# Kernel optimization log

Measured on AMD Instinct MI355X. Metric: run time of the kernel, lower is better.

Reference implementation:

```python
import jax, jax.numpy as jnp
import numpy as np
import math

H = 16          # num_heads
EPS = 1e-5      # LayerNorm eps (torch default)


def setup_inputs() -> dict:
    key = jax.random.key(0)
    ks = jax.random.split(key, 4)
    B, T, D = 2, 2048, 1024
    s = 1.0 / math.sqrt(D)
    return {
        "x": jax.random.normal(ks[0], (B, T, D), dtype=jnp.float32),
        "ln_g": jnp.ones((D,), jnp.float32),
        "ln_b": jnp.zeros((D,), jnp.float32),
        "Wq": jax.random.normal(ks[1], (D, D), jnp.float32) * s,
        "bq": jnp.zeros((D,), jnp.float32),
        "Wk": jax.random.normal(ks[2], (D, D), jnp.float32) * s,
        "bk": jnp.zeros((D,), jnp.float32),
        "Wv": jax.random.normal(ks[3], (D, D), jnp.float32) * s,
        "bv": jnp.zeros((D,), jnp.float32),
    }


def reference(x, ln_g, ln_b, Wq, bq, Wk, bk, Wv, bv):
    B, T, D = x.shape
    # LayerNorm (shared across the three projections, computed once)
    mu = jnp.mean(x, axis=-1, keepdims=True)
    var = jnp.mean(jnp.square(x - mu), axis=-1, keepdims=True)
    xn = (x - mu) * jax.lax.rsqrt(var + EPS) * ln_g + ln_b
    # Q/K/V projections -> [B, T, H, Dh]
    q = (xn @ Wq + bq).reshape(B, T, H, D // H)
    k = (xn @ Wk + bk).reshape(B, T, H, D // H)
    v = (xn @ Wv + bv).reshape(B, T, H, D // H)
    # QK^T scores [B, n, m, h], scaled by sqrt(head_dim)
    scale = 1.0 / math.sqrt(D // H)
    attn = jnp.einsum('bnhd,bmhd->bnmh', q, k) * scale
    # softmax over key axis (dim=2), dropout p=0 is identity
    w = jax.nn.softmax(attn, axis=2)
    # weighted sum of values, merge heads
    y = jnp.einsum('bnmh,bmhd->bnhd', w, v).reshape(B, T, D)
    return y
```

## Files before the change

kernel.cpp:

```cpp
#include <hip/hip_runtime.h>
#include <hip/hip_bf16.h>


typedef __attribute__((ext_vector_type(8)))  short short8;
typedef __attribute__((ext_vector_type(4)))  float f32x4;
typedef __attribute__((ext_vector_type(2)))  float f32x2;
typedef __attribute__((ext_vector_type(16))) float f32x16;
typedef __attribute__((ext_vector_type(2)))  unsigned int uint2v;

#define D_MODEL 1024
#define T_SEQ   2048
#define NHEAD   16
#define HDIM    64

#define LOG2E 1.4426950408889634f

__device__ __forceinline__ unsigned short f2bf(float x) {
    unsigned int u = __float_as_uint(x);
    u = (u + 0x7fffu + ((u >> 16) & 1u)) >> 16;
    return (unsigned short)u;
}

#if defined(__has_builtin)
#if __has_builtin(__builtin_amdgcn_permlane32_swap)
#define HAVE_PERMSWAP 1
#endif
#endif

__device__ __forceinline__ uint2v permswap(unsigned a, unsigned b) {
#ifdef HAVE_PERMSWAP
    return __builtin_amdgcn_permlane32_swap(a, b, false, false);
#else
    uint2v r;
    const unsigned as = (unsigned)__shfl_xor((int)a, 32, 64);
    const unsigned bs = (unsigned)__shfl_xor((int)b, 32, 64);
    const bool hi = (threadIdx.x & 32) != 0;
    r[0] = hi ? bs : a;
    r[1] = hi ? b  : as;
    return r;
#endif
}

__device__ __forceinline__ void w8(unsigned short* p, const uint4 v) {
    uint2 a; a.x = v.x; a.y = v.y;
    uint2 b; b.x = v.z; b.y = v.w;
    *(uint2*)p = a;
    *(uint2*)(p + 4) = b;
}

__device__ __forceinline__ short8 read8(const unsigned short* p) {
    union { unsigned u[4]; short8 s; } r;
    const uint2 a = *(const uint2*)p;
    const uint2 b = *(const uint2*)(p + 4);
    r.u[0] = a.x; r.u[1] = a.y; r.u[2] = b.x; r.u[3] = b.y;
    return r.s;
}

__global__ __launch_bounds__(256) void ln_kernel(
    const float* __restrict__ x, const float* __restrict__ gam,
    const float* __restrict__ bet, unsigned short* __restrict__ xn)
{
    const int row = blockIdx.x;
    const int t = threadIdx.x;
    const float4 v = ((const float4*)(x + (size_t)row * D_MODEL))[t];
    float s  = v.x + v.y + v.z + v.w;
    float s2 = v.x * v.x + v.y * v.y + v.z * v.z + v.w * v.w;
#pragma unroll
    for (int off = 32; off; off >>= 1) {
        s  += __shfl_down(s,  off, 64);
        s2 += __shfl_down(s2, off, 64);
    }
    __shared__ float red[8];
    const int lane = t & 63, wave = t >> 6;
    if (lane == 0) { red[wave] = s; red[4 + wave] = s2; }
    __syncthreads();
    s  = red[0] + red[1] + red[2] + red[3];
    s2 = red[4] + red[5] + red[6] + red[7];
    const float mu   = s * (1.f / D_MODEL);
    const float var  = s2 * (1.f / D_MODEL) - mu * mu;
    const float rstd = rsqrtf(var + 1e-5f);
    const float4 gv = ((const float4*)gam)[t];
    const float4 bv = ((const float4*)bet)[t];
    ushort4 o;
    o.x = f2bf((v.x - mu) * rstd * gv.x + bv.x);
    o.y = f2bf((v.y - mu) * rstd * gv.y + bv.y);
    o.z = f2bf((v.z - mu) * rstd * gv.z + bv.z);
    o.w = f2bf((v.w - mu) * rstd * gv.w + bv.w);
    ((ushort4*)(xn + (size_t)row * D_MODEL))[t] = o;
}

__global__ __launch_bounds__(256) void wcast_kernel(
    const float* __restrict__ Wq, const float* __restrict__ Wk,
    const float* __restrict__ Wv, unsigned short* __restrict__ Wt)
{
    const float* W = (blockIdx.z == 0) ? Wq : (blockIdx.z == 1) ? Wk : Wv;
    unsigned short* out = Wt + (size_t)blockIdx.z * D_MODEL * D_MODEL;
    __shared__ float tile[32][33];
    const int n0 = blockIdx.x * 32, k0 = blockIdx.y * 32;
#pragma unroll
    for (int i = threadIdx.y; i < 32; i += 8)
        tile[i][threadIdx.x] = W[(size_t)(k0 + i) * D_MODEL + n0 + threadIdx.x];
    __syncthreads();
#pragma unroll
    for (int i = threadIdx.y; i < 32; i += 8)
        out[(size_t)(n0 + i) * D_MODEL + k0 + threadIdx.x] = f2bf(tile[threadIdx.x][i]);
}

__global__ __launch_bounds__(256) void qkv_gemm_kernel(
    const unsigned short* __restrict__ xn, const unsigned short* __restrict__ Wt,
    const float* __restrict__ bq, const float* __restrict__ bk, const float* __restrict__ bv,
    unsigned short* __restrict__ qo, unsigned short* __restrict__ ko, unsigned short* __restrict__ vo)
{
    const int which = blockIdx.x >> 3;
    const unsigned short* Bw = Wt + (size_t)which * (D_MODEL * D_MODEL);
    const float* bias   = (which == 0) ? bq : (which == 1) ? bk : bv;
    unsigned short* out = (which == 0) ? qo : (which == 1) ? ko : vo;
    const float scale   = (which == 0) ? (0.125f * LOG2E) : 1.0f;
    const int m0 = blockIdx.y * 128, n0 = (blockIdx.x & 7) * 128;

    __shared__ unsigned short As[128][32];
    __shared__ unsigned short Bs[128][32];

    const int tid = threadIdx.x;
    const int lane = tid & 63, wave = tid >> 6;
    const int wr = wave >> 1, wc = wave & 1;
    const int g = lane >> 4, c = lane & 15;

    const int srow = (lane >> 2);
    const int scol = (lane & 3) * 8;

    f32x4 acc[4][4] = {};

    for (int kt = 0; kt < D_MODEL; kt += 32) {
        __syncthreads();
#pragma unroll
        for (int i = 0; i < 2; ++i) {
            const int r = wave * 32 + i * 16;
            const unsigned short* ga = xn + (size_t)(m0 + r + srow) * D_MODEL + kt + scol;
            __builtin_amdgcn_global_load_lds(
                (const __attribute__((address_space(1))) unsigned int*)ga,
                (__attribute__((address_space(3))) unsigned int*)(&As[r][0]), 16, 0, 0);
            const unsigned short* gb = Bw + (size_t)(n0 + r + srow) * D_MODEL + kt + scol;
            __builtin_amdgcn_global_load_lds(
                (const __attribute__((address_space(1))) unsigned int*)gb,
                (__attribute__((address_space(3))) unsigned int*)(&Bs[r][0]), 16, 0, 0);
        }
        __syncthreads();

        short8 af[4], bf[4];
#pragma unroll
        for (int i = 0; i < 4; ++i) {
            af[i] = *(const short8*)(&As[wr * 64 + i * 16 + c][g * 8]);
            bf[i] = *(const short8*)(&Bs[wc * 64 + i * 16 + c][g * 8]);
        }
#pragma unroll
        for (int i = 0; i < 4; ++i)
#pragma unroll
            for (int j = 0; j < 4; ++j)
                acc[i][j] = __builtin_amdgcn_mfma_f32_16x16x32_bf16(af[i], bf[j], acc[i][j], 0, 0, 0);
    }

#pragma unroll
    for (int j = 0; j < 4; ++j) {
        const int n = n0 + wc * 64 + j * 16 + c;
        const float bn = bias[n];
        const int h = n >> 6, dh = n & 63;
#pragma unroll
        for (int i = 0; i < 4; ++i) {
#pragma unroll
            for (int r = 0; r < 4; ++r) {
                const int m = m0 + wr * 64 + i * 16 + g * 4 + r;
                const int bb = m >> 11, t = m & 2047;
                out[((size_t)(bb * NHEAD + h) * T_SEQ + t) * HDIM + dh] =
                    f2bf((acc[i][j][r] + bn) * scale);
            }
        }
    }
}

__global__ __launch_bounds__(256) void vtrans_kernel(
    const unsigned short* __restrict__ vh, unsigned short* __restrict__ vt)
{
    __shared__ unsigned short tile[64][65];
    const int t0 = blockIdx.x * 64;
    const int bh = blockIdx.y;
    const unsigned short* src = vh + (size_t)bh * T_SEQ * HDIM;
    unsigned short* dst = vt + (size_t)bh * HDIM * T_SEQ;
    const int r0 = threadIdx.x >> 3, d0 = (threadIdx.x & 7) * 8;
#pragma unroll
    for (int it = 0; it < 2; ++it) {
        const int r = r0 + it * 32;
        const uint4 v = *(const uint4*)(src + (size_t)(t0 + r) * HDIM + d0);
        const unsigned short* vs = (const unsigned short*)&v;
#pragma unroll
        for (int j = 0; j < 8; ++j) tile[r][d0 + j] = vs[j];
    }
    __syncthreads();
#pragma unroll
    for (int it = 0; it < 2; ++it) {
        const int dh = r0 + it * 32;
        unsigned short tmp[8];
#pragma unroll
        for (int j = 0; j < 8; ++j) tmp[j] = tile[d0 + j][dh];
        *(uint4*)(dst + (size_t)dh * T_SEQ + t0 + d0) = *(const uint4*)tmp;
    }
}

__global__ __launch_bounds__(512, 4) void attn_kernel(
    const unsigned short* __restrict__ qb, const unsigned short* __restrict__ kb,
    const unsigned short* __restrict__ vtb, float* __restrict__ out)
{
    const int id  = blockIdx.x;
    const int swz = (id & 7) * 64 + (id >> 3);
    const int qt  = swz & 15;
    const int bh  = swz >> 4;
    const int b = bh >> 4, head = bh & 15;
    const unsigned short* Q  = qb  + (size_t)bh * T_SEQ * HDIM;
    const unsigned short* Kp = kb  + (size_t)bh * T_SEQ * HDIM;
    const unsigned short* Vt = vtb + (size_t)bh * HDIM * T_SEQ;

    __shared__ __align__(16) unsigned short smem[34816];

    const int tid = threadIdx.x, lane = tid & 63, wave = tid >> 6;
    const int grp = wave >> 2, w4 = wave & 3;
    const int q = lane & 31, h = lane >> 5;
    const int kvbase = grp * (T_SEQ / 2);

    const int gtid = tid & 255;
    const int sr = gtid >> 3;
    const int sc = (gtid & 7) * 8;

    unsigned short* gbase = &smem[grp * 17408];

    short8 qf[4];
    {
        const unsigned short* qp = Q + (size_t)(qt * 128 + w4 * 32 + q) * HDIM;
#pragma unroll
        for (int c = 0; c < 4; ++c)
            qf[c] = *(const short8*)(qp + c * 16 + h * 8);
    }

    float l_r = 0.f;
    f32x16 o[2] = {};

    const unsigned short* kp0 = Kp + (size_t)(kvbase + sr) * HDIM + sc;
    const unsigned short* vp0 = Vt + (size_t)sr * T_SEQ + kvbase + sc;
    uint4 kr0 = *(const uint4*)(kp0);
    uint4 kr1 = *(const uint4*)(kp0 + 32 * HDIM);
    uint4 vr0 = *(const uint4*)(vp0);
    uint4 vr1 = *(const uint4*)(vp0 + 32 * T_SEQ);
    w8(gbase + sr * 68 + sc, kr0);
    w8(gbase + (sr + 32) * 68 + sc, kr1);
    w8(gbase + 8704 + sr * 68 + sc, vr0);
    w8(gbase + 8704 + (sr + 32) * 68 + sc, vr1);
    kp0 += 64 * HDIM;
    vp0 += 64;

    int cur = 0;
#pragma unroll 1
    for (int t = 0; t < 16; ++t) {
        const bool more = (t + 1 < 16);
        if (more) {
            kr0 = *(const uint4*)(kp0);
            kr1 = *(const uint4*)(kp0 + 32 * HDIM);
            vr0 = *(const uint4*)(vp0);
            vr1 = *(const uint4*)(vp0 + 32 * T_SEQ);
            kp0 += 64 * HDIM;
            vp0 += 64;
        }
        __syncthreads();
        const unsigned short* kbuf = gbase + cur * 4352;
        const unsigned short* vbuf = gbase + 8704 + cur * 4352;

        f32x16 s0 = {}, s1 = {};
        __builtin_amdgcn_s_setprio(1);
#pragma unroll
        for (int c = 0; c < 4; ++c) {
            const short8 kf0 = read8(kbuf + (size_t)q * 68 + c * 16 + h * 8);
            const short8 kf1 = read8(kbuf + (size_t)(32 + q) * 68 + c * 16 + h * 8);
            s0 = __builtin_amdgcn_mfma_f32_32x32x16_bf16(kf0, qf[c], s0, 0, 0, 0);
            s1 = __builtin_amdgcn_mfma_f32_32x32x16_bf16(kf1, qf[c], s1, 0, 0, 0);
        }
        __builtin_amdgcn_s_setprio(0);

#pragma unroll
        for (int r = 0; r < 16; ++r) { s0[r] = exp2f(s0[r]); }
#pragma unroll
        for (int r = 0; r < 16; ++r) { s1[r] = exp2f(s1[r]); }

        {
            f32x2 u[8];
#pragma unroll
            for (int r = 0; r < 8; ++r) {
                f32x2 a; a[0] = s0[2*r]; a[1] = s0[2*r+1];
                f32x2 bb; bb[0] = s1[2*r]; bb[1] = s1[2*r+1];
                u[r] = a + bb;
            }
            u[0] += u[1]; u[2] += u[3]; u[4] += u[5]; u[6] += u[7];
            u[0] += u[2]; u[4] += u[6];
            u[0] += u[4];
            float rs = u[0][0] + u[0][1];
            rs += __shfl_xor(rs, 32, 64);
            l_r += rs;
        }

        unsigned Wb0[8], Wb1[8];
#pragma unroll
        for (int u = 0; u < 4; ++u) {
            asm("v_cvt_pk_bf16_f32 %0, %1, %2" : "=v"(Wb0[u*2])   : "v"(s0[4*u]),   "v"(s0[4*u+1]));
            asm("v_cvt_pk_bf16_f32 %0, %1, %2" : "=v"(Wb0[u*2+1]) : "v"(s0[4*u+2]), "v"(s0[4*u+3]));
            asm("v_cvt_pk_bf16_f32 %0, %1, %2" : "=v"(Wb1[u*2])   : "v"(s1[4*u]),   "v"(s1[4*u+1]));
            asm("v_cvt_pk_bf16_f32 %0, %1, %2" : "=v"(Wb1[u*2+1]) : "v"(s1[4*u+2]), "v"(s1[4*u+3]));
        }

        short8 pf[4];
#pragma unroll
        for (int m = 0; m < 2; ++m) {
            {
                const uint2v r0 = permswap(Wb0[4*m],     Wb0[4*m + 2]);
                const uint2v r1 = permswap(Wb0[4*m + 1], Wb0[4*m + 3]);
                union { unsigned u[4]; short8 s; } pw;
                pw.u[0] = r0[0]; pw.u[1] = r1[0]; pw.u[2] = r0[1]; pw.u[3] = r1[1];
                pf[m] = pw.s;
            }
            {
                const uint2v r0 = permswap(Wb1[4*m],     Wb1[4*m + 2]);
                const uint2v r1 = permswap(Wb1[4*m + 1], Wb1[4*m + 3]);
                union { unsigned u[4]; short8 s; } pw;
                pw.u[0] = r0[0]; pw.u[1] = r1[0]; pw.u[2] = r0[1]; pw.u[3] = r1[1];
                pf[2 + m] = pw.s;
            }
        }

        __builtin_amdgcn_s_setprio(1);
#pragma unroll
        for (int dt = 0; dt < 2; ++dt) {
#pragma unroll
            for (int cp = 0; cp < 4; ++cp) {
                const short8 vf = read8(vbuf + (size_t)(dt * 32 + q) * 68 + cp * 16 + h * 8);
                o[dt] = __builtin_amdgcn_mfma_f32_32x32x16_bf16(vf, pf[cp], o[dt], 0, 0, 0);
            }
        }
        __builtin_amdgcn_s_setprio(0);

        if (more) {
            unsigned short* kd = gbase + (cur ^ 1) * 4352;
            unsigned short* vd = gbase + 8704 + (cur ^ 1) * 4352;
            w8(kd + sr * 68 + sc, kr0);
            w8(kd + (sr + 32) * 68 + sc, kr1);
            w8(vd + sr * 68 + sc, vr0);
            w8(vd + (sr + 32) * 68 + sc, vr1);
        }
        cur ^= 1;
    }

    __syncthreads();
    float* obuf  = (float*)(void*)smem;
    float* l_lds = ((float*)(void*)smem) + 128 * 68;

    const int qrl = w4 * 32 + q;
    if (grp == 0) {
#pragma unroll
        for (int dt = 0; dt < 2; ++dt)
#pragma unroll
            for (int u = 0; u < 4; ++u) {
                float* dst = obuf + (size_t)qrl * 68 + dt * 32 + 8 * u + 4 * h;
                float2 lo; lo.x = o[dt][4*u];     lo.y = o[dt][4*u + 1];
                float2 hi; hi.x = o[dt][4*u + 2]; hi.y = o[dt][4*u + 3];
                *(float2*)dst = lo;
                *(float2*)(dst + 2) = hi;
            }
        if (h == 0) l_lds[qrl] = l_r;
    }
    __syncthreads();
    if (grp == 1) {
        const float invl = 1.0f / (l_lds[qrl] + l_r);
#pragma unroll
        for (int dt = 0; dt < 2; ++dt)
#pragma unroll
            for (int u = 0; u < 4; ++u) {
                float* dst = obuf + (size_t)qrl * 68 + dt * 32 + 8 * u + 4 * h;
                float2 lo = *(const float2*)dst;
                float2 hi = *(const float2*)(dst + 2);
                lo.x = (lo.x + o[dt][4*u])     * invl;
                lo.y = (lo.y + o[dt][4*u + 1]) * invl;
                hi.x = (hi.x + o[dt][4*u + 2]) * invl;
                hi.y = (hi.y + o[dt][4*u + 3]) * invl;
                *(float2*)dst = lo;
                *(float2*)(dst + 2) = hi;
            }
    }
    __syncthreads();
#pragma unroll
    for (int it = 0; it < 4; ++it) {
        const int row = it * 32 + (tid >> 4);
        const int col = (tid & 15) * 4;
        const float4 v = *(const float4*)(&obuf[(size_t)row * 68 + col]);
        *(float4*)(&out[(size_t)(b * T_SEQ + qt * 128 + row) * D_MODEL + head * HDIM + col]) = v;
    }
}

extern "C" void kernel_launch(void* const* d_in, const int* in_sizes, int n_in,
                              void* d_out, int out_size, void* d_ws, size_t ws_size,
                              hipStream_t stream)
{
    const float* x   = (const float*)d_in[0];
    const float* lng = (const float*)d_in[1];
    const float* lnb = (const float*)d_in[2];
    const float* Wq  = (const float*)d_in[3];
    const float* bq  = (const float*)d_in[4];
    const float* Wk  = (const float*)d_in[5];
    const float* bk  = (const float*)d_in[6];
    const float* Wv  = (const float*)d_in[7];
    const float* bv  = (const float*)d_in[8];
    float* out = (float*)d_out;

    unsigned short* xn = (unsigned short*)d_ws;
    unsigned short* Wt = xn + (size_t)4096 * 1024;
    unsigned short* qh = Wt + (size_t)3 * 1024 * 1024;
    unsigned short* kh = qh + (size_t)4096 * 1024;
    unsigned short* vh = kh + (size_t)4096 * 1024;
    unsigned short* vt = xn;

    ln_kernel<<<4096, 256, 0, stream>>>(x, lng, lnb, xn);
    wcast_kernel<<<dim3(32, 32, 3), dim3(32, 8), 0, stream>>>(Wq, Wk, Wv, Wt);
    qkv_gemm_kernel<<<dim3(24, 32), 256, 0, stream>>>(xn, Wt, bq, bk, bv, qh, kh, vh);
    vtrans_kernel<<<dim3(32, 32), 256, 0, stream>>>(vh, vt);
    attn_kernel<<<512, 512, 0, stream>>>(qh, kh, vt, out);
}
```

Measured before the change: 111.9 us.

## Fuse LN with weight cast, emit transposed V from GEMM, use group barrier

Merges the LayerNorm and weight-cast kernels into one launch. For the V projection the GEMM now swaps its operands (W_v^T times xn^T), so it writes V directly in the head-dim-major layout the attention kernel reads, and the separate transpose kernel is removed. The attention loop's __syncthreads is replaced with an explicit lgkmcnt wait followed by s_barrier. Together these cut two kernel launches and one round trip of V through memory. The V epilogue now writes along t with per-element stores, which may be less coalesced.

```diff
diff --git a/kernel.cpp b/kernel.cpp
--- a/kernel.cpp
+++ b/kernel.cpp
@@ -41,6 +41,12 @@
 #endif
 }
 
+__device__ __forceinline__ void group_barrier() {
+    asm volatile("s_waitcnt lgkmcnt(0)" ::: "memory");
+    __builtin_amdgcn_s_barrier();
+    asm volatile("" ::: "memory");
+}
+
 __device__ __forceinline__ void w8(unsigned short* p, const uint4 v) {
     uint2 a; a.x = v.x; a.y = v.y;
     uint2 b; b.x = v.z; b.y = v.w;
@@ -56,67 +62,74 @@
     return r.s;
 }
 
-__global__ __launch_bounds__(256) void ln_kernel(
+__global__ __launch_bounds__(256) void ln_wcast_kernel(
     const float* __restrict__ x, const float* __restrict__ gam,
-    const float* __restrict__ bet, unsigned short* __restrict__ xn)
-{
-    const int row = blockIdx.x;
-    const int t = threadIdx.x;
-    const float4 v = ((const float4*)(x + (size_t)row * D_MODEL))[t];
-    float s  = v.x + v.y + v.z + v.w;
-    float s2 = v.x * v.x + v.y * v.y + v.z * v.z + v.w * v.w;
-#pragma unroll
-    for (int off = 32; off; off >>= 1) {
-        s  += __shfl_down(s,  off, 64);
-        s2 += __shfl_down(s2, off, 64);
-    }
-    __shared__ float red[8];
-    const int lane = t & 63, wave = t >> 6;
-    if (lane == 0) { red[wave] = s; red[4 + wave] = s2; }
-    __syncthreads();
-    s  = red[0] + red[1] + red[2] + red[3];
-    s2 = red[4] + red[5] + red[6] + red[7];
-    const float mu   = s * (1.f / D_MODEL);
-    const float var  = s2 * (1.f / D_MODEL) - mu * mu;
-    const float rstd = rsqrtf(var + 1e-5f);
-    const float4 gv = ((const float4*)gam)[t];
-    const float4 bv = ((const float4*)bet)[t];
-    ushort4 o;
-    o.x = f2bf((v.x - mu) * rstd * gv.x + bv.x);
-    o.y = f2bf((v.y - mu) * rstd * gv.y + bv.y);
-    o.z = f2bf((v.z - mu) * rstd * gv.z + bv.z);
-    o.w = f2bf((v.w - mu) * rstd * gv.w + bv.w);
-    ((ushort4*)(xn + (size_t)row * D_MODEL))[t] = o;
-}
-
-__global__ __launch_bounds__(256) void wcast_kernel(
+    const float* __restrict__ bet, unsigned short* __restrict__ xn,
     const float* __restrict__ Wq, const float* __restrict__ Wk,
     const float* __restrict__ Wv, unsigned short* __restrict__ Wt)
 {
-    const float* W = (blockIdx.z == 0) ? Wq : (blockIdx.z == 1) ? Wk : Wv;
-    unsigned short* out = Wt + (size_t)blockIdx.z * D_MODEL * D_MODEL;
+    __shared__ float red[8];
     __shared__ float tile[32][33];
-    const int n0 = blockIdx.x * 32, k0 = blockIdx.y * 32;
-#pragma unroll
-    for (int i = threadIdx.y; i < 32; i += 8)
-        tile[i][threadIdx.x] = W[(size_t)(k0 + i) * D_MODEL + n0 + threadIdx.x];
-    __syncthreads();
-#pragma unroll
-    for (int i = threadIdx.y; i < 32; i += 8)
-        out[(size_t)(n0 + i) * D_MODEL + k0 + threadIdx.x] = f2bf(tile[threadIdx.x][i]);
+    const int bid = blockIdx.x;
+    if (bid < 4096) {
+        const int row = bid;
+        const int t = threadIdx.x;
+        const float4 v = ((const float4*)(x + (size_t)row * D_MODEL))[t];
+        float s  = v.x + v.y + v.z + v.w;
+        float s2 = v.x * v.x + v.y * v.y + v.z * v.z + v.w * v.w;
+#pragma unroll
+        for (int off = 32; off; off >>= 1) {
+            s  += __shfl_down(s,  off, 64);
+            s2 += __shfl_down(s2, off, 64);
+        }
+        const int lane = t & 63, wave = t >> 6;
+        if (lane == 0) { red[wave] = s; red[4 + wave] = s2; }
+        __syncthreads();
+        s  = red[0] + red[1] + red[2] + red[3];
+        s2 = red[4] + red[5] + red[6] + red[7];
+        const float mu   = s * (1.f / D_MODEL);
+        const float var  = s2 * (1.f / D_MODEL) - mu * mu;
+        const float rstd = rsqrtf(var + 1e-5f);
+        const float4 gv = ((const float4*)gam)[t];
+        const float4 bv = ((const float4*)bet)[t];
+        ushort4 o;
+        o.x = f2bf((v.x - mu) * rstd * gv.x + bv.x);
+        o.y = f2bf((v.y - mu) * rstd * gv.y + bv.y);
+        o.z = f2bf((v.z - mu) * rstd * gv.z + bv.z);
+        o.w = f2bf((v.w - mu) * rstd * gv.w + bv.w);
+        ((ushort4*)(xn + (size_t)row * D_MODEL))[t] = o;
+    } else {
+        const int id = bid - 4096;
+        const int z  = id >> 10;
+        const int t2 = id & 1023;
+        const int n0 = (t2 & 31) * 32, k0 = (t2 >> 5) * 32;
+        const float* W = (z == 0) ? Wq : (z == 1) ? Wk : Wv;
+        unsigned short* outw = Wt + (size_t)z * D_MODEL * D_MODEL;
+        const int tx = threadIdx.x & 31, ty = threadIdx.x >> 5;
+#pragma unroll
+        for (int i = ty; i < 32; i += 8)
+            tile[i][tx] = W[(size_t)(k0 + i) * D_MODEL + n0 + tx];
+        __syncthreads();
+#pragma unroll
+        for (int i = ty; i < 32; i += 8)
+            outw[(size_t)(n0 + i) * D_MODEL + k0 + tx] = f2bf(tile[tx][i]);
+    }
 }
 
 __global__ __launch_bounds__(256) void qkv_gemm_kernel(
     const unsigned short* __restrict__ xn, const unsigned short* __restrict__ Wt,
     const float* __restrict__ bq, const float* __restrict__ bk, const float* __restrict__ bv,
-    unsigned short* __restrict__ qo, unsigned short* __restrict__ ko, unsigned short* __restrict__ vo)
+    unsigned short* __restrict__ qo, unsigned short* __restrict__ ko, unsigned short* __restrict__ vt)
 {
     const int which = blockIdx.x >> 3;
-    const unsigned short* Bw = Wt + (size_t)which * (D_MODEL * D_MODEL);
+    const int xt = blockIdx.x & 7, yt = blockIdx.y;
+    const bool vmode = (which == 2);
+    const unsigned short* Aptr = vmode ? (Wt + (size_t)2 * D_MODEL * D_MODEL) : xn;
+    const unsigned short* Bptr = vmode ? xn : (Wt + (size_t)which * D_MODEL * D_MODEL);
     const float* bias   = (which == 0) ? bq : (which == 1) ? bk : bv;
-    unsigned short* out = (which == 0) ? qo : (which == 1) ? ko : vo;
     const float scale   = (which == 0) ? (0.125f * LOG2E) : 1.0f;
-    const int m0 = blockIdx.y * 128, n0 = (blockIdx.x & 7) * 128;
+    const int m0 = vmode ? xt * 128 : yt * 128;
+    const int n0 = vmode ? yt * 128 : xt * 128;
 
     __shared__ unsigned short As[128][32];
     __shared__ unsigned short Bs[128][32];
@@ -136,11 +149,11 @@
 #pragma unroll
         for (int i = 0; i < 2; ++i) {
             const int r = wave * 32 + i * 16;
-            const unsigned short* ga = xn + (size_t)(m0 + r + srow) * D_MODEL + kt + scol;
+            const unsigned short* ga = Aptr + (size_t)(m0 + r + srow) * D_MODEL + kt + scol;
             __builtin_amdgcn_global_load_lds(
                 (const __attribute__((address_space(1))) unsigned int*)ga,
                 (__attribute__((address_space(3))) unsigned int*)(&As[r][0]), 16, 0, 0);
-            const unsigned short* gb = Bw + (size_t)(n0 + r + srow) * D_MODEL + kt + scol;
+            const unsigned short* gb = Bptr + (size_t)(n0 + r + srow) * D_MODEL + kt + scol;
             __builtin_amdgcn_global_load_lds(
                 (const __attribute__((address_space(1))) unsigned int*)gb,
                 (__attribute__((address_space(3))) unsigned int*)(&Bs[r][0]), 16, 0, 0);
@@ -160,49 +173,40 @@
                 acc[i][j] = __builtin_amdgcn_mfma_f32_16x16x32_bf16(af[i], bf[j], acc[i][j], 0, 0, 0);
     }
 
-#pragma unroll
-    for (int j = 0; j < 4; ++j) {
-        const int n = n0 + wc * 64 + j * 16 + c;
-        const float bn = bias[n];
-        const int h = n >> 6, dh = n & 63;
+    if (!vmode) {
+        unsigned short* out = (which == 0) ? qo : ko;
+#pragma unroll
+        for (int j = 0; j < 4; ++j) {
+            const int n = n0 + wc * 64 + j * 16 + c;
+            const float bn = bias[n];
+            const int h = n >> 6, dh = n & 63;
+#pragma unroll
+            for (int i = 0; i < 4; ++i) {
+#pragma unroll
+                for (int r = 0; r < 4; ++r) {
+                    const int m = m0 + wr * 64 + i * 16 + g * 4 + r;
+                    const int bb = m >> 11, t = m & 2047;
+                    out[((size_t)(bb * NHEAD + h) * T_SEQ + t) * HDIM + dh] =
+                        f2bf((acc[i][j][r] + bn) * scale);
+                }
+            }
+        }
+    } else {
 #pragma unroll
         for (int i = 0; i < 4; ++i) {
 #pragma unroll
             for (int r = 0; r < 4; ++r) {
                 const int m = m0 + wr * 64 + i * 16 + g * 4 + r;
-                const int bb = m >> 11, t = m & 2047;
-                out[((size_t)(bb * NHEAD + h) * T_SEQ + t) * HDIM + dh] =
-                    f2bf((acc[i][j][r] + bn) * scale);
-            }
-        }
-    }
-}
-
-__global__ __launch_bounds__(256) void vtrans_kernel(
-    const unsigned short* __restrict__ vh, unsigned short* __restrict__ vt)
-{
-    __shared__ unsigned short tile[64][65];
-    const int t0 = blockIdx.x * 64;
-    const int bh = blockIdx.y;
-    const unsigned short* src = vh + (size_t)bh * T_SEQ * HDIM;
-    unsigned short* dst = vt + (size_t)bh * HDIM * T_SEQ;
-    const int r0 = threadIdx.x >> 3, d0 = (threadIdx.x & 7) * 8;
-#pragma unroll
-    for (int it = 0; it < 2; ++it) {
-        const int r = r0 + it * 32;
-        const uint4 v = *(const uint4*)(src + (size_t)(t0 + r) * HDIM + d0);
-        const unsigned short* vs = (const unsigned short*)&v;
-#pragma unroll
-        for (int j = 0; j < 8; ++j) tile[r][d0 + j] = vs[j];
-    }
-    __syncthreads();
-#pragma unroll
-    for (int it = 0; it < 2; ++it) {
-        const int dh = r0 + it * 32;
-        unsigned short tmp[8];
-#pragma unroll
-        for (int j = 0; j < 8; ++j) tmp[j] = tile[d0 + j][dh];
-        *(uint4*)(dst + (size_t)dh * T_SEQ + t0 + d0) = *(const uint4*)tmp;
+                const float bn = bias[m];
+#pragma unroll
+                for (int j = 0; j < 4; ++j) {
+                    const int n = n0 + wc * 64 + j * 16 + c;
+                    const int bb = n >> 11, t = n & 2047;
+                    vt[(size_t)bb * (D_MODEL * T_SEQ) + (size_t)m * T_SEQ + t] =
+                        f2bf(acc[i][j][r] + bn);
+                }
+            }
+        }
     }
 }
 
@@ -217,7 +221,8 @@
     const int b = bh >> 4, head = bh & 15;
     const unsigned short* Q  = qb  + (size_t)bh * T_SEQ * HDIM;
     const unsigned short* Kp = kb  + (size_t)bh * T_SEQ * HDIM;
-    const unsigned short* Vt = vtb + (size_t)bh * HDIM * T_SEQ;
+    const unsigned short* Vt = vtb + (size_t)b * (D_MODEL * T_SEQ)
+                                   + (size_t)head * (HDIM * T_SEQ);
 
     __shared__ __align__(16) unsigned short smem[34816];
 
@@ -268,7 +273,7 @@
             kp0 += 64 * HDIM;
             vp0 += 64;
         }
-        __syncthreads();
+        group_barrier();
         const unsigned short* kbuf = gbase + cur * 4352;
         const unsigned short* vbuf = gbase + 8704 + cur * 4352;
 
@@ -419,12 +424,9 @@
     unsigned short* Wt = xn + (size_t)4096 * 1024;
     unsigned short* qh = Wt + (size_t)3 * 1024 * 1024;
     unsigned short* kh = qh + (size_t)4096 * 1024;
-    unsigned short* vh = kh + (size_t)4096 * 1024;
-    unsigned short* vt = xn;
-
-    ln_kernel<<<4096, 256, 0, stream>>>(x, lng, lnb, xn);
-    wcast_kernel<<<dim3(32, 32, 3), dim3(32, 8), 0, stream>>>(Wq, Wk, Wv, Wt);
-    qkv_gemm_kernel<<<dim3(24, 32), 256, 0, stream>>>(xn, Wt, bq, bk, bv, qh, kh, vh);
-    vtrans_kernel<<<dim3(32, 32), 256, 0, stream>>>(vh, vt);
+    unsigned short* vt = kh + (size_t)4096 * 1024;
+
+    ln_wcast_kernel<<<7168, 256, 0, stream>>>(x, lng, lnb, xn, Wq, Wk, Wv, Wt);
+    qkv_gemm_kernel<<<dim3(24, 32), 256, 0, stream>>>(xn, Wt, bq, bk, bv, qh, kh, vt);
     attn_kernel<<<512, 512, 0, stream>>>(qh, kh, vt, out);
 }
```

Result: no change. 112.0 us (+0.1%).
